# Performance work log

Hardware: AMD Instinct MI355X
Metric: run time of the kernel (lower is better)

Reference implementation:

```python
import jax, jax.numpy as jnp
import numpy as np

DIM = 1024
HEADS = 16
DIM_HEAD = 64
INNER = HEADS * DIM_HEAD  # 1024
SCALE = DIM_HEAD ** -0.5


def setup_inputs() -> dict:
    key = jax.random.key(0)
    ks = jax.random.split(key, 7)
    b, n = 4, 1024
    x = jax.random.normal(ks[0], (b, n, DIM), dtype=jnp.float32)
    # Dense kernels (glorot-ish scale), mix-head matrices are N(0,1) as in source
    Wq = jax.random.normal(ks[1], (DIM, INNER), dtype=jnp.float32) * (DIM ** -0.5)
    Wkv = jax.random.normal(ks[2], (DIM, 2 * INNER), dtype=jnp.float32) * (DIM ** -0.5)
    mix_pre = jax.random.normal(ks[3], (HEADS, HEADS), dtype=jnp.float32)
    mix_post = jax.random.normal(ks[4], (HEADS, HEADS), dtype=jnp.float32)
    Wo = jax.random.normal(ks[5], (INNER, DIM), dtype=jnp.float32) * (INNER ** -0.5)
    bo = jnp.zeros((DIM,), dtype=jnp.float32)
    return {"x": x, "Wq": Wq, "Wkv": Wkv, "mix_pre": mix_pre,
            "mix_post": mix_post, "Wo": Wo, "bo": bo}


def reference(x, Wq, Wkv, mix_pre, mix_post, Wo, bo):
    b, n, _ = x.shape
    # context = x (self-attention path)
    q = x @ Wq                      # [b, n, inner]
    kv = x @ Wkv                    # [b, n, 2*inner]
    k, v = jnp.split(kv, 2, axis=-1)
    split_heads = lambda t: t.reshape(b, n, HEADS, DIM_HEAD).transpose(0, 2, 1, 3)
    q, k, v = map(split_heads, (q, k, v))  # [b, h, n, d]
    dots = jnp.einsum('bhid,bhjd->bhij', q, k) * SCALE
    dots = jnp.einsum('bhij,hg->bgij', dots, mix_pre)   # talking-heads pre-softmax
    attn = jax.nn.softmax(dots, axis=-1)
    attn = jnp.einsum('bhij,hg->bgij', attn, mix_post)  # talking-heads post-softmax
    out = jnp.einsum('bhij,bhjd->bhid', attn, v)        # [b, h, n, d]
    out = out.transpose(0, 2, 1, 3).reshape(b, n, INNER)
    return out @ Wo + bo            # dropout rate 0 -> identity
```

## Files before the change

kernel.cpp:

```cpp
#include <hip/hip_runtime.h>
#include <hip/hip_bf16.h>

using bf16 = __hip_bfloat16;

typedef __bf16 bf16x8 __attribute__((ext_vector_type(8)));
typedef __bf16 bf16x2v __attribute__((ext_vector_type(2)));
typedef float  f32x4  __attribute__((ext_vector_type(4)));
typedef float  f32x2  __attribute__((ext_vector_type(2)));

#define QK_SCALE 0.125f

__device__ __forceinline__ void load_lds16(const bf16* g, bf16* l) {
  __builtin_amdgcn_global_load_lds(
      (const __attribute__((address_space(1))) unsigned int*)g,
      (__attribute__((address_space(3))) unsigned int*)l, 16, 0, 0);
}

__device__ __forceinline__ unsigned pack_bf2(float a, float b) {
  bf16x2v v;
  v[0] = (__bf16)a;
  v[1] = (__bf16)b;
  return __builtin_bit_cast(unsigned, v);
}

struct alignas(8) bf16x4s { bf16 a, b, c, d; };

__global__ __launch_bounds__(256)
void prep_k(const float* __restrict__ x, bf16x4s* __restrict__ xb,
            const float* __restrict__ Wq, const float* __restrict__ Wkv,
            const float* __restrict__ Wo,
            bf16* __restrict__ WT, bf16* __restrict__ WoT)
{
  const int bid = blockIdx.x;
  const int tid = threadIdx.x;

  if (bid >= 4096) {
    const int i = (bid - 4096) * 256 + tid;
    const float4 v = ((const float4*)x)[i];
    xb[i] = { (bf16)v.x, (bf16)v.y, (bf16)v.z, (bf16)v.w };
    return;
  }

  __shared__ bf16 t[32][33];
  const float* in;
  bf16* out;
  int ldi, c0, r0;
  if (bid < 1024)      { in = Wq;  out = WT;           ldi = 1024;
                         c0 = (bid & 31) * 32;        r0 = (bid >> 5) * 32; }
  else if (bid < 3072) { const int lb = bid - 1024;
                         in = Wkv; out = WT + 1048576; ldi = 2048;
                         c0 = (lb % 64) * 32;          r0 = (lb / 64) * 32; }
  else                 { const int lb = bid - 3072;
                         in = Wo;  out = WoT;          ldi = 1024;
                         c0 = (lb & 31) * 32;          r0 = (lb >> 5) * 32; }
  const int xx = tid & 31, yy = tid >> 5;
#pragma unroll
  for (int dy = 0; dy < 32; dy += 8)
    t[yy + dy][xx] = (bf16)in[(long)(r0 + yy + dy) * ldi + c0 + xx];
  __syncthreads();
#pragma unroll
  for (int dy = 0; dy < 32; dy += 8)
    out[(long)(c0 + yy + dy) * 1024 + r0 + xx] = t[xx][yy + dy];
}

template<int TM, int TN, int WM, int WN, bool BIAS, typename CT>
__global__ __launch_bounds__(256, 2)
void gemm_nt(const bf16* __restrict__ A, const bf16* __restrict__ B,
             CT* __restrict__ C, const float* __restrict__ bias,
             int K, int lda, int ldb, int ldc,
             long sA0, long sA1, long sB0, long sB1, long sC0, long sC1,
             int nz1, float alpha)
{
  constexpr int BK = 64;
  constexpr int LDE = TN + 8;
  constexpr unsigned SB_STAGE = (TM + TN) * BK * 2;
  constexpr unsigned SB_EP = (sizeof(CT) == 2) ? TM * LDE * 2 : 0;
  constexpr unsigned SBYTES = SB_STAGE > SB_EP ? SB_STAGE : SB_EP;
  __shared__ __align__(16) char smem[SBYTES];
  bf16* lsA = (bf16*)smem;
  bf16* lsB = lsA + TM * BK;

  const int z = blockIdx.z;
  A += (long)(z / nz1) * sA0 + (long)(z % nz1) * sA1;
  B += (long)(z / nz1) * sB0 + (long)(z % nz1) * sB1;
  C += (long)(z / nz1) * sC0 + (long)(z % nz1) * sC1;
  const int tm0 = blockIdx.y * TM;
  const int tn0 = blockIdx.x * TN;

  const int tid = threadIdx.x;
  const int w = tid >> 6, l = tid & 63;
  constexpr int WCOLS = TN / WN;
  const int wm = (w / WCOLS) * WM, wn = (w % WCOLS) * WN;
  constexpr int AM = WM / 16, AN = WN / 16;
  f32x4 acc[AM][AN] = {};
  const int kg = l >> 4, rl = l & 15;

  constexpr int RA = TM / 32, RB = TN / 32;
  const int srow0 = tid >> 3;
  const int schunk = tid & 7;

  for (int k0 = 0; k0 < K; k0 += BK) {
#pragma unroll
    for (int r = 0; r < RA; ++r) {
      const int row = r * 32 + srow0;
      const int sw = ((row >> 1) & 7) ^ ((row & 1) << 2);
      const int col8 = schunk ^ sw;
      load_lds16(A + (long)(tm0 + row) * lda + (k0 + col8 * 8),
                 &lsA[row * BK + schunk * 8]);
    }
#pragma unroll
    for (int r = 0; r < RB; ++r) {
      const int row = r * 32 + srow0;
      const int sw = ((row >> 1) & 7) ^ ((row & 1) << 2);
      const int col8 = schunk ^ sw;
      load_lds16(B + (long)(tn0 + row) * ldb + (k0 + col8 * 8),
                 &lsB[row * BK + schunk * 8]);
    }
    __syncthreads();

#pragma unroll
    for (int half = 0; half < 2; ++half) {
      bf16x8 af[AM], bfr[AN];
#pragma unroll
      for (int i = 0; i < AM; ++i) {
        const int m = wm + i * 16 + rl;
        const int sw = ((m >> 1) & 7) ^ ((m & 1) << 2);
        const int p = (half * 4 + kg) ^ sw;
        af[i] = *(const bf16x8*)&lsA[m * BK + p * 8];
      }
#pragma unroll
      for (int j = 0; j < AN; ++j) {
        const int n = wn + j * 16 + rl;
        const int sw = ((n >> 1) & 7) ^ ((n & 1) << 2);
        const int p = (half * 4 + kg) ^ sw;
        bfr[j] = *(const bf16x8*)&lsB[n * BK + p * 8];
      }
#pragma unroll
      for (int i = 0; i < AM; ++i)
#pragma unroll
        for (int j = 0; j < AN; ++j)
          acc[i][j] = __builtin_amdgcn_mfma_f32_16x16x32_bf16(af[i], bfr[j], acc[i][j], 0, 0, 0);
    }
    __syncthreads();
  }

  if constexpr (sizeof(CT) == 2) {
    bf16* ep = (bf16*)smem;
#pragma unroll
    for (int i = 0; i < AM; ++i) {
#pragma unroll
      for (int j = 0; j < AN; ++j) {
        const int col = wn + j * 16 + rl;
        float bv = 0.f;
        if (BIAS) bv = bias[tn0 + col];
#pragma unroll
        for (int v = 0; v < 4; ++v) {
          const int row = wm + i * 16 + (l >> 4) * 4 + v;
          ep[row * LDE + col] = (bf16)(acc[i][j][v] * alpha + bv);
        }
      }
    }
    __syncthreads();
    constexpr int CH = (TM * TN) / 2048;
#pragma unroll
    for (int c = 0; c < CH; ++c) {
      const int gidx = (c * 256 + tid) * 8;
      const int row = gidx / TN, col = gidx % TN;
      *(uint4*)&C[(long)(tm0 + row) * ldc + tn0 + col] = *(const uint4*)&ep[row * LDE + col];
    }
  } else {
#pragma unroll
    for (int i = 0; i < AM; ++i) {
#pragma unroll
      for (int j = 0; j < AN; ++j) {
        const int col = tn0 + wn + j * 16 + rl;
        float bv = 0.f;
        if (BIAS) bv = bias[col];
#pragma unroll
        for (int v = 0; v < 4; ++v) {
          const int row = tm0 + wm + i * 16 + (l >> 4) * 4 + v;
          C[(long)row * ldc + col] = (CT)(acc[i][j][v] * alpha + bv);
        }
      }
    }
  }
}

__global__ __launch_bounds__(256)
void mix_softmax_mix(bf16* __restrict__ S,
                     const float* __restrict__ mixpre, const float* __restrict__ mixpost)
{
  constexpr int LDJ = 1028;
  __shared__ __align__(16) unsigned int lSp[8 * LDJ];
  __shared__ float pre[256], post[256];
  __shared__ float redZ[4][16];
  const int i = blockIdx.x, b = blockIdx.y;
  const int tid = threadIdx.x;
  pre[tid]  = mixpre[tid];
  post[tid] = mixpost[tid];
  const long hstr = 1048576L;
  bf16* Srow = S + (long)b * 16 * hstr + (long)i * 1024;
  const int w = tid >> 6, l = tid & 63;
  const int rl = l & 15, q = l >> 4;

#pragma unroll
  for (int r = 0; r < 4; ++r) {
    const int u = r * 256 + tid;
    const int h2 = u >> 7, jg = (u & 127) * 8;
    const uint4 a  = *(const uint4*)&Srow[(long)(2 * h2)     * hstr + jg];
    const uint4 c4 = *(const uint4*)&Srow[(long)(2 * h2 + 1) * hstr + jg];
    uint4 w0, w1;
    w0.x = (a.x & 0xFFFFu) | (c4.x << 16);
    w0.y = (a.x >> 16)     | (c4.x & 0xFFFF0000u);
    w0.z = (a.y & 0xFFFFu) | (c4.y << 16);
    w0.w = (a.y >> 16)     | (c4.y & 0xFFFF0000u);
    w1.x = (a.z & 0xFFFFu) | (c4.z << 16);
    w1.y = (a.z >> 16)     | (c4.z & 0xFFFF0000u);
    w1.z = (a.w & 0xFFFFu) | (c4.w << 16);
    w1.w = (a.w >> 16)     | (c4.w & 0xFFFF0000u);
    *(uint4*)&lSp[h2 * LDJ + jg]     = w0;
    *(uint4*)&lSp[h2 * LDJ + jg + 4] = w1;
  }
  __syncthreads();

  bf16x8 aHi, aLo;
#pragma unroll
  for (int e = 0; e < 8; ++e) {
    const int h = q * 8 + e;
    const float c = (h < 16) ? pre[(h & 15) * 16 + rl] : 0.f;
    const __bf16 hi = (__bf16)c;
    aHi[e] = hi;
    aLo[e] = (__bf16)(c - (float)hi);
  }

  const int hq2 = (q & 1) * 4;
  const int cw = w * 256;

  unsigned ph01[16], ph23[16];
  f32x4 zac = {0.f, 0.f, 0.f, 0.f};
#pragma unroll
  for (int c = 0; c < 16; ++c) {
    const int col = cw + c * 16 + rl;
    uint4 bw;
    bw.x = lSp[(hq2 + 0) * LDJ + col];
    bw.y = lSp[(hq2 + 1) * LDJ + col];
    bw.z = lSp[(hq2 + 2) * LDJ + col];
    bw.w = lSp[(hq2 + 3) * LDJ + col];
    const bf16x8 bfr = __builtin_bit_cast(bf16x8, bw);
    f32x4 d = __builtin_amdgcn_mfma_f32_16x16x32_bf16(aHi, bfr, f32x4{0.f,0.f,0.f,0.f}, 0, 0, 0);
    d = __builtin_amdgcn_mfma_f32_16x16x32_bf16(aLo, bfr, d, 0, 0, 0);
    float ev[4];
#pragma unroll
    for (int v = 0; v < 4; ++v) {
      ev[v] = __expf(d[v] - 10.f);
      zac[v] += ev[v];
    }
    ph01[c] = pack_bf2(ev[0], ev[1]);
    ph23[c] = pack_bf2(ev[2], ev[3]);
  }
#pragma unroll
  for (int off = 1; off < 16; off <<= 1) {
#pragma unroll
    for (int v = 0; v < 4; ++v) zac[v] += __shfl_xor(zac[v], off, 64);
  }
  if (rl == 0) {
#pragma unroll
    for (int v = 0; v < 4; ++v) redZ[w][q * 4 + v] = zac[v];
  }
  __syncthreads();

  bf16x8 pHi, pLo;
#pragma unroll
  for (int e = 0; e < 8; ++e) {
    const int g = q * 8 + e;
    float c = 0.f;
    if (g < 16) {
      const float Z = redZ[0][g & 15] + redZ[1][g & 15] + redZ[2][g & 15] + redZ[3][g & 15];
      c = post[(g & 15) * 16 + rl] / Z;
    }
    const __bf16 hi = (__bf16)c;
    pHi[e] = hi;
    pLo[e] = (__bf16)(c - (float)hi);
  }

  const int src0 = rl + 32 * (q & 1);
  const int src1 = src0 + 16;
#pragma unroll
  for (int c = 0; c < 16; ++c) {
    const unsigned d0 = (unsigned)__shfl((int)ph01[c], src0, 64);
    const unsigned d1 = (unsigned)__shfl((int)ph23[c], src0, 64);
    const unsigned d2 = (unsigned)__shfl((int)ph01[c], src1, 64);
    const unsigned d3 = (unsigned)__shfl((int)ph23[c], src1, 64);
    uint4 raw = {d0, d1, d2, d3};
    bf16x8 bfr = *(const bf16x8*)&raw;
    f32x4 d = __builtin_amdgcn_mfma_f32_16x16x32_bf16(pHi, bfr, f32x4{0.f,0.f,0.f,0.f}, 0, 0, 0);
    d = __builtin_amdgcn_mfma_f32_16x16x32_bf16(pLo, bfr, d, 0, 0, 0);
    const int col = cw + c * 16 + rl;
#pragma unroll
    for (int v = 0; v < 4; ++v)
      Srow[(long)(q * 4 + v) * hstr + col] = (bf16)d[v];
  }
}

extern "C" void kernel_launch(void* const* d_in, const int* in_sizes, int n_in,
                              void* d_out, int out_size, void* d_ws, size_t ws_size,
                              hipStream_t stream)
{
  const float* x     = (const float*)d_in[0];
  const float* Wq    = (const float*)d_in[1];
  const float* Wkv   = (const float*)d_in[2];
  const float* mpre  = (const float*)d_in[3];
  const float* mpost = (const float*)d_in[4];
  const float* Wo    = (const float*)d_in[5];
  const float* bo    = (const float*)d_in[6];
  float* out = (float*)d_out;

  char* ws = (char*)d_ws;
  const size_t MB = 1024 * 1024;
  if (ws_size < 184 * MB) return;
  bf16* xb   = (bf16*)(ws);
  bf16* QKV  = (bf16*)(ws + 8 * MB);
  bf16* WT   = (bf16*)(ws + 32 * MB);
  bf16* WoT  = (bf16*)(ws + 38 * MB);
  bf16* VT   = (bf16*)(ws + 40 * MB);
  bf16* Obuf = (bf16*)(ws + 48 * MB);
  bf16* Sbuf = (bf16*)(ws + 56 * MB);

  prep_k<<<8192, 256, 0, stream>>>(x, (bf16x4s*)xb, Wq, Wkv, Wo, WT, WoT);

  gemm_nt<128, 128, 64, 64, false, bf16><<<dim3(16, 32, 1), 256, 0, stream>>>(
      xb, WT, QKV, nullptr, 1024, 1024, 1024, 3072, 0, 0, 0, 0, 0, 0, 1, 1.f);

  gemm_nt<64, 128, 32, 64, false, bf16><<<dim3(8, 1, 64), 256, 0, stream>>>(
      WT + 2097152, xb, VT, nullptr, 1024, 1024, 1024, 1024,
      0, 65536, 1048576, 0, 1048576, 65536, 16, 1.f);

  gemm_nt<128, 128, 64, 64, false, bf16><<<dim3(8, 8, 64), 256, 0, stream>>>(
      QKV, QKV + 1024, Sbuf, nullptr, 64, 3072, 3072, 1024,
      3145728, 64, 3145728, 64, 16L * 1048576, 1048576, 16, QK_SCALE);

  mix_softmax_mix<<<dim3(1024, 4, 1), 256, 0, stream>>>(Sbuf, mpre, mpost);

  gemm_nt<128, 64, 64, 32, false, bf16><<<dim3(1, 8, 64), 256, 0, stream>>>(
      Sbuf, VT, Obuf, nullptr, 1024, 1024, 1024, 1024,
      16L * 1048576, 1048576, 16L * 65536, 65536, 1048576, 64, 16, 1.f);

  gemm_nt<128, 128, 64, 64, true, float><<<dim3(8, 32, 1), 256, 0, stream>>>(
      Obuf, WoT, out, bo, 1024, 1024, 1024, 1024, 0, 0, 0, 0, 0, 0, 1, 1.f);
}
```

Before: 259.8 us.

## Merge QKV and V-transpose GEMMs into one launch; reuse Q tile in QK kernel

The QKV projection GEMM and the transposed-V GEMM are merged into one kernel launch that dispatches by block index to a shared device-side GEMM body. The QK^T GEMM is replaced by a dedicated kernel where each block loads its 128-row Q tile once and loops over all eight K column tiles, reloading only K. The aim is to cut launch overhead, fill the GPU better by co-scheduling the two projection GEMMs, and avoid reloading Q. The trade-off is a longer serial loop per QK block, now only 512 blocks, with no double buffering across K tiles.

```diff
diff --git a/kernel.cpp b/kernel.cpp
--- a/kernel.cpp
+++ b/kernel.cpp
@@ -64,28 +64,15 @@
 }
 
 template<int TM, int TN, int WM, int WN, bool BIAS, typename CT>
-__global__ __launch_bounds__(256, 2)
-void gemm_nt(const bf16* __restrict__ A, const bf16* __restrict__ B,
-             CT* __restrict__ C, const float* __restrict__ bias,
-             int K, int lda, int ldb, int ldc,
-             long sA0, long sA1, long sB0, long sB1, long sC0, long sC1,
-             int nz1, float alpha)
+__device__ __forceinline__
+void gemm_body(char* smem, const bf16* __restrict__ A, const bf16* __restrict__ B,
+               CT* __restrict__ C, const float* __restrict__ bias,
+               int K, int lda, int ldb, int ldc, int tm0, int tn0, float alpha)
 {
   constexpr int BK = 64;
   constexpr int LDE = TN + 8;
-  constexpr unsigned SB_STAGE = (TM + TN) * BK * 2;
-  constexpr unsigned SB_EP = (sizeof(CT) == 2) ? TM * LDE * 2 : 0;
-  constexpr unsigned SBYTES = SB_STAGE > SB_EP ? SB_STAGE : SB_EP;
-  __shared__ __align__(16) char smem[SBYTES];
   bf16* lsA = (bf16*)smem;
   bf16* lsB = lsA + TM * BK;
-
-  const int z = blockIdx.z;
-  A += (long)(z / nz1) * sA0 + (long)(z % nz1) * sA1;
-  B += (long)(z / nz1) * sB0 + (long)(z % nz1) * sB1;
-  C += (long)(z / nz1) * sC0 + (long)(z % nz1) * sC1;
-  const int tm0 = blockIdx.y * TM;
-  const int tn0 = blockIdx.x * TN;
 
   const int tid = threadIdx.x;
   const int w = tid >> 6, l = tid & 63;
@@ -168,6 +155,7 @@
       const int row = gidx / TN, col = gidx % TN;
       *(uint4*)&C[(long)(tm0 + row) * ldc + tn0 + col] = *(const uint4*)&ep[row * LDE + col];
     }
+    __syncthreads();
   } else {
 #pragma unroll
     for (int i = 0; i < AM; ++i) {
@@ -183,6 +171,139 @@
         }
       }
     }
+  }
+}
+
+template<int TM, int TN, int WM, int WN, bool BIAS, typename CT>
+__global__ __launch_bounds__(256, 2)
+void gemm_nt(const bf16* __restrict__ A, const bf16* __restrict__ B,
+             CT* __restrict__ C, const float* __restrict__ bias,
+             int K, int lda, int ldb, int ldc,
+             long sA0, long sA1, long sB0, long sB1, long sC0, long sC1,
+             int nz1, float alpha)
+{
+  constexpr int BK = 64;
+  constexpr int LDE = TN + 8;
+  constexpr unsigned SB_STAGE = (TM + TN) * BK * 2;
+  constexpr unsigned SB_EP = (sizeof(CT) == 2) ? TM * LDE * 2 : 0;
+  constexpr unsigned SBYTES = SB_STAGE > SB_EP ? SB_STAGE : SB_EP;
+  __shared__ __align__(16) char smem[SBYTES];
+
+  const int z = blockIdx.z;
+  A += (long)(z / nz1) * sA0 + (long)(z % nz1) * sA1;
+  B += (long)(z / nz1) * sB0 + (long)(z % nz1) * sB1;
+  C += (long)(z / nz1) * sC0 + (long)(z % nz1) * sC1;
+  gemm_body<TM, TN, WM, WN, BIAS, CT>(smem, A, B, C, bias, K, lda, ldb, ldc,
+                                      blockIdx.y * TM, blockIdx.x * TN, alpha);
+}
+
+__global__ __launch_bounds__(256, 2)
+void projvt_k(const bf16* __restrict__ xb, const bf16* __restrict__ WT,
+              bf16* __restrict__ QKV, bf16* __restrict__ VT)
+{
+  __shared__ __align__(16) char smem[34816];
+  const int bid = blockIdx.x;
+  if (bid < 512) {
+    gemm_body<128, 128, 64, 64, false, bf16>(smem, xb, WT, QKV, nullptr,
+        1024, 1024, 1024, 3072, (bid >> 4) * 128, (bid & 15) * 128, 1.f);
+  } else {
+    const int lb = bid - 512;
+    const int xt = lb & 7, z = lb >> 3;
+    const int b2 = z >> 4, gp = z & 15;
+    gemm_body<64, 128, 32, 64, false, bf16>(smem,
+        WT + 2097152 + (long)gp * 65536,
+        xb + (long)b2 * 1048576,
+        VT + (long)b2 * 1048576 + (long)gp * 65536, nullptr,
+        1024, 1024, 1024, 1024, 0, xt * 128, 1.f);
+  }
+}
+
+__global__ __launch_bounds__(256, 2)
+void qk_j(const bf16* __restrict__ QKV, bf16* __restrict__ S)
+{
+  constexpr int BK = 64;
+  __shared__ __align__(16) bf16 lsA[128 * BK];
+  __shared__ __align__(16) bf16 lsB[128 * BK];
+  const int z = blockIdx.z;
+  const int b = z >> 4, h = z & 15;
+  const bf16* Q  = QKV + (long)b * 3145728 + h * 64;
+  const bf16* Kp = QKV + (long)b * 3145728 + 1024 + h * 64;
+  bf16* C = S + (long)z * 1048576;
+  const int tm0 = blockIdx.x * 128;
+
+  const int tid = threadIdx.x;
+  const int w = tid >> 6, l = tid & 63;
+  const int wm = (w >> 1) * 64, wn = (w & 1) * 64;
+  const int kg = l >> 4, rl = l & 15;
+  const int srow0 = tid >> 3, schunk = tid & 7;
+
+#pragma unroll
+  for (int r = 0; r < 4; ++r) {
+    const int row = r * 32 + srow0;
+    const int sw = ((row >> 1) & 7) ^ ((row & 1) << 2);
+    const int col8 = schunk ^ sw;
+    load_lds16(Q + (long)(tm0 + row) * 3072 + col8 * 8, &lsA[row * BK + schunk * 8]);
+  }
+#pragma unroll
+  for (int r = 0; r < 4; ++r) {
+    const int row = r * 32 + srow0;
+    const int sw = ((row >> 1) & 7) ^ ((row & 1) << 2);
+    const int col8 = schunk ^ sw;
+    load_lds16(Kp + (long)row * 3072 + col8 * 8, &lsB[row * BK + schunk * 8]);
+  }
+  __syncthreads();
+
+  for (int t = 0; t < 8; ++t) {
+    if (t > 0) {
+      __syncthreads();
+#pragma unroll
+      for (int r = 0; r < 4; ++r) {
+        const int row = r * 32 + srow0;
+        const int sw = ((row >> 1) & 7) ^ ((row & 1) << 2);
+        const int col8 = schunk ^ sw;
+        load_lds16(Kp + (long)(t * 128 + row) * 3072 + col8 * 8,
+                   &lsB[row * BK + schunk * 8]);
+      }
+      __syncthreads();
+    }
+
+    f32x4 acc[4][4] = {};
+#pragma unroll
+    for (int half = 0; half < 2; ++half) {
+      bf16x8 af[4], bfr[4];
+#pragma unroll
+      for (int i = 0; i < 4; ++i) {
+        const int m = wm + i * 16 + rl;
+        const int sw = ((m >> 1) & 7) ^ ((m & 1) << 2);
+        const int p = (half * 4 + kg) ^ sw;
+        af[i] = *(const bf16x8*)&lsA[m * BK + p * 8];
+      }
+#pragma unroll
+      for (int j = 0; j < 4; ++j) {
+        const int n = wn + j * 16 + rl;
+        const int sw = ((n >> 1) & 7) ^ ((n & 1) << 2);
+        const int p = (half * 4 + kg) ^ sw;
+        bfr[j] = *(const bf16x8*)&lsB[n * BK + p * 8];
+      }
+#pragma unroll
+      for (int i = 0; i < 4; ++i)
+#pragma unroll
+        for (int j = 0; j < 4; ++j)
+          acc[i][j] = __builtin_amdgcn_mfma_f32_16x16x32_bf16(af[i], bfr[j], acc[i][j], 0, 0, 0);
+    }
+
+    const int tn0 = t * 128;
+#pragma unroll
+    for (int i = 0; i < 4; ++i)
+#pragma unroll
+      for (int j = 0; j < 4; ++j) {
+        const int col = tn0 + wn + j * 16 + rl;
+#pragma unroll
+        for (int v = 0; v < 4; ++v) {
+          const int row = tm0 + wm + i * 16 + kg * 4 + v;
+          C[(long)row * 1024 + col] = (bf16)(acc[i][j][v] * QK_SCALE);
+        }
+      }
   }
 }
 
@@ -328,16 +449,9 @@
 
   prep_k<<<8192, 256, 0, stream>>>(x, (bf16x4s*)xb, Wq, Wkv, Wo, WT, WoT);
 
-  gemm_nt<128, 128, 64, 64, false, bf16><<<dim3(16, 32, 1), 256, 0, stream>>>(
-      xb, WT, QKV, nullptr, 1024, 1024, 1024, 3072, 0, 0, 0, 0, 0, 0, 1, 1.f);
-
-  gemm_nt<64, 128, 32, 64, false, bf16><<<dim3(8, 1, 64), 256, 0, stream>>>(
-      WT + 2097152, xb, VT, nullptr, 1024, 1024, 1024, 1024,
-      0, 65536, 1048576, 0, 1048576, 65536, 16, 1.f);
-
-  gemm_nt<128, 128, 64, 64, false, bf16><<<dim3(8, 8, 64), 256, 0, stream>>>(
-      QKV, QKV + 1024, Sbuf, nullptr, 64, 3072, 3072, 1024,
-      3145728, 64, 3145728, 64, 16L * 1048576, 1048576, 16, QK_SCALE);
+  projvt_k<<<1024, 256, 0, stream>>>(xb, WT, QKV, VT);
+
+  qk_j<<<dim3(8, 1, 64), 256, 0, stream>>>(QKV, Sbuf);
 
   mix_softmax_mix<<<dim3(1024, 4, 1), 256, 0, stream>>>(Sbuf, mpre, mpost);
 
```

New measurement: 249.6 us. 3.9% less time.
